# Performance work log

Measured on AMD Instinct MI355X. Metric: run time of the kernel, lower is better.

The kernel has to match this reference:

```python
import jax, jax.numpy as jnp
import numpy as np

N_NODES = 100000


def setup_inputs() -> dict:
    key = jax.random.key(0)
    k1, k2, k3 = jax.random.split(key, 3)
    x = jax.random.normal(k1, (N_NODES, 128), dtype=jnp.float32)
    edge_index = jax.random.randint(k2, (2, 1600000), 0, N_NODES, dtype=jnp.int64)
    # PyG GCNConv internal Linear (glorot init approximated by scaled normal), bias zeros
    W = jax.random.normal(k3, (128, 128), dtype=jnp.float32) * (1.0 / np.sqrt(128.0))
    b = jnp.zeros((128,), dtype=jnp.float32)
    return {"x": x, "edge_index": edge_index, "W": W, "b": b}


def gcn_conv(x, edge_index, W, b):
    N = x.shape[0]
    # add self loops
    loop = jnp.arange(N, dtype=edge_index.dtype)
    src = jnp.concatenate([edge_index[0], loop])  # message sources
    dst = jnp.concatenate([edge_index[1], loop])  # aggregation targets
    # symmetric normalization D^{-1/2} (A + I) D^{-1/2}; degree counted at dst (PyG default)
    ones = jnp.ones(src.shape[0], dtype=x.dtype)
    deg = jax.ops.segment_sum(ones, dst, num_segments=N)
    deg_inv_sqrt = jnp.where(deg > 0, jax.lax.rsqrt(jnp.maximum(deg, 1.0)), 0.0)
    norm = deg_inv_sqrt[src] * deg_inv_sqrt[dst]  # [E+N]
    h = x @ W  # [N, out]
    msgs = h[src] * norm[:, None]  # gather + scale, [E+N, out]
    agg = jax.ops.segment_sum(msgs, dst, num_segments=N)  # scatter-add
    return agg + b


def reference(x, edge_index, W, b):
    # GCNConvSC: residual + GCNConv
    return x + gcn_conv(x, edge_index, W, b)
```

## Files before the change

kernel.cpp:

```cpp
#include <hip/hip_runtime.h>


typedef __attribute__((ext_vector_type(8))) short short8;
typedef __attribute__((ext_vector_type(4))) float floatx4;

__device__ inline unsigned bf16rne(float f) {
    unsigned u = __builtin_bit_cast(unsigned, f);
    return (u + 0x7FFFu + ((u >> 16) & 1u)) >> 16;
}
__device__ inline unsigned pack2(float lo, float hi) {
    return bf16rne(lo) | (bf16rne(hi) << 16);
}
__device__ inline float bflo(unsigned u) { return __builtin_bit_cast(float, u << 16); }
__device__ inline float bfhi(unsigned u) { return __builtin_bit_cast(float, u & 0xFFFF0000u); }

#define NPB   128
#define MAXNB 1024
#define SRCB  17
#define SRCMASK ((1u << SRCB) - 1u)

__global__ void k_cvt(const float* __restrict__ x, const float* __restrict__ dis,
                      char* __restrict__ outc, int N) {
    int t = blockIdx.x * blockDim.x + threadIdx.x;
    if (t >= N * 16) return;
    int r = t >> 4, g = t & 15;
    float d = dis[r];
    const float* p = x + (size_t)r * 128 + g * 8;
    float4 a = *(const float4*)p;
    float4 c = *(const float4*)(p + 4);
    uint4 v;
    v.x = pack2(d * a.x, d * a.y); v.y = pack2(d * a.z, d * a.w);
    v.z = pack2(d * c.x, d * c.y); v.w = pack2(d * c.z, d * c.w);
    *(uint4*)(outc + (size_t)r * 512 + 256 + g * 16) = v;
}

__global__ __launch_bounds__(256) void k_hist(const int* __restrict__ dst,
                                              int* __restrict__ hist,
                                              int E, int NB, int NBLK, int chunk) {
    __shared__ int h[MAXNB];
    int tid = threadIdx.x, b = blockIdx.x;
    for (int i = tid; i < NB; i += 256) h[i] = 0;
    __syncthreads();
    int e0 = b * chunk, e1 = min(e0 + chunk, E);
    for (int e = e0 + tid; e < e1; e += 256) atomicAdd(&h[dst[e] >> 7], 1);
    __syncthreads();
    for (int k = tid; k < NB; k += 256) hist[(size_t)k * NBLK + b] = h[k];
}

__global__ __launch_bounds__(256) void k_part(const int* __restrict__ a,
                                              int* __restrict__ part, int M) {
    __shared__ int sums[256];
    int tid = threadIdx.x;
    int base = blockIdx.x * 1024 + tid * 4;
    int s = 0;
#pragma unroll
    for (int k = 0; k < 4; ++k) { int i = base + k; if (i < M) s += a[i]; }
    sums[tid] = s;
    __syncthreads();
    for (int off = 128; off > 0; off >>= 1) {
        if (tid < off) sums[tid] += sums[tid + off];
        __syncthreads();
    }
    if (tid == 0) part[blockIdx.x] = sums[0];
}

__global__ __launch_bounds__(256) void k_mid(int* __restrict__ part,
                                             int* __restrict__ ptrN,
                                             int nblk, int E) {
    __shared__ int s[256];
    int tid = threadIdx.x;
    s[tid] = (tid < nblk) ? part[tid] : 0;
    __syncthreads();
    for (int off = 1; off < 256; off <<= 1) {
        int v = (tid >= off) ? s[tid - off] : 0;
        __syncthreads();
        s[tid] += v;
        __syncthreads();
    }
    if (tid < nblk) part[tid] = tid ? s[tid - 1] : 0;
    if (tid == 0) ptrN[0] = E;
}

__global__ __launch_bounds__(256) void k_applyg(const int* __restrict__ a,
                                                const int* __restrict__ part,
                                                int* __restrict__ out, int M) {
    __shared__ int sums[256];
    int tid = threadIdx.x;
    int base = blockIdx.x * 1024 + tid * 4;
    int c[4];
    int s = 0;
#pragma unroll
    for (int k = 0; k < 4; ++k) {
        int i = base + k;
        c[k] = (i < M) ? a[i] : 0;
        s += c[k];
    }
    sums[tid] = s;
    __syncthreads();
    for (int off = 1; off < 256; off <<= 1) {
        int v = (tid >= off) ? sums[tid - off] : 0;
        __syncthreads();
        sums[tid] += v;
        __syncthreads();
    }
    int run = part[blockIdx.x] + (tid ? sums[tid - 1] : 0);
#pragma unroll
    for (int k = 0; k < 4; ++k) {
        int i = base + k;
        if (i < M) { out[i] = run; run += c[k]; }
    }
}

__global__ __launch_bounds__(256) void k_scat(const int* __restrict__ ei,
                                              const int* __restrict__ base,
                                              unsigned* __restrict__ packed,
                                              int E, int NB, int NBLK, int chunk) {
    __shared__ int fill[MAXNB];
    int tid = threadIdx.x, b = blockIdx.x;
    for (int k = tid; k < NB; k += 256) fill[k] = base[(size_t)k * NBLK + b];
    __syncthreads();
    int e0 = b * chunk, e1 = min(e0 + chunk, E);
    for (int e = e0 + tid; e < e1; e += 256) {
        int s = ei[e];
        int d = ei[E + e];
        int pos = atomicAdd(&fill[d >> 7], 1);
        packed[pos] = (unsigned)s | ((unsigned)(d & (NPB - 1)) << SRCB);
    }
}

__global__ __launch_bounds__(256) void k_sort(const unsigned* __restrict__ packed,
                                              const int* __restrict__ base,
                                              int* __restrict__ csr_src,
                                              int* __restrict__ ptr,
                                              float* __restrict__ dis,
                                              int E, int NB, int NBLK, int N) {
    __shared__ int cnt[NPB], scn[NPB], fill[NPB];
    int tid = threadIdx.x, k = blockIdx.x;
    int s0 = base[(size_t)k * NBLK];
    int s1 = (k + 1 < NB) ? base[(size_t)(k + 1) * NBLK] : E;
    if (tid < NPB) cnt[tid] = 0;
    __syncthreads();
    for (int j = s0 + tid; j < s1; j += 256) atomicAdd(&cnt[packed[j] >> SRCB], 1);
    __syncthreads();
    if (tid < NPB) scn[tid] = cnt[tid];
    __syncthreads();
    for (int off = 1; off < NPB; off <<= 1) {
        int v = (tid < NPB && tid >= off) ? scn[tid - off] : 0;
        __syncthreads();
        if (tid < NPB) scn[tid] += v;
        __syncthreads();
    }
    if (tid < NPB) {
        int excl = scn[tid] - cnt[tid];
        fill[tid] = excl;
        int gn = k * NPB + tid;
        if (gn < N) {
            ptr[gn] = s0 + excl;
            dis[gn] = rsqrtf((float)(cnt[tid] + 1));
        }
    }
    __syncthreads();
    for (int j = s0 + tid; j < s1; j += 256) {
        unsigned p = packed[j];
        int loc = atomicAdd(&fill[p >> SRCB], 1);
        csr_src[s0 + loc] = (int)(p & SRCMASK);
    }
}

#define ACC8(v)                         \
    do {                                \
        acc[0] += bflo((v).x);          \
        acc[1] += bfhi((v).x);          \
        acc[2] += bflo((v).y);          \
        acc[3] += bfhi((v).y);          \
        acc[4] += bflo((v).z);          \
        acc[5] += bfhi((v).z);          \
        acc[6] += bflo((v).w);          \
        acc[7] += bfhi((v).w);          \
    } while (0)

__global__ __launch_bounds__(256) void k_gather(char* __restrict__ outc,
                                                const int* __restrict__ csr_src,
                                                const int* __restrict__ ptr,
                                                const float* __restrict__ dis,
                                                int N) {
    int lane = threadIdx.x & 63;
    int q = lane >> 4, sub = lane & 15;
    int node = (blockIdx.x * blockDim.x + threadIdx.x) >> 6;
    if (node >= N) return;
    int lo = ptr[node], hi = ptr[node + 1];
    float dd = dis[node];
    const char* xb = outc + 256 + (size_t)sub * 16;

    float acc[8] = {0.f, 0.f, 0.f, 0.f, 0.f, 0.f, 0.f, 0.f};

    if (q == 0) {
        uint4 v = *(const uint4*)(xb + (size_t)node * 512);
        ACC8(v);
    }
    int j = lo + q;
    for (; j + 12 < hi; j += 16) {
        int s0 = csr_src[j];
        int s1 = csr_src[j + 4];
        int s2 = csr_src[j + 8];
        int s3 = csr_src[j + 12];
        uint4 v0 = *(const uint4*)(xb + (size_t)s0 * 512);
        uint4 v1 = *(const uint4*)(xb + (size_t)s1 * 512);
        uint4 v2 = *(const uint4*)(xb + (size_t)s2 * 512);
        uint4 v3 = *(const uint4*)(xb + (size_t)s3 * 512);
        ACC8(v0);
        ACC8(v1);
        ACC8(v2);
        ACC8(v3);
    }
    for (; j + 4 < hi; j += 8) {
        int s0 = csr_src[j];
        int s1 = csr_src[j + 4];
        uint4 v0 = *(const uint4*)(xb + (size_t)s0 * 512);
        uint4 v1 = *(const uint4*)(xb + (size_t)s1 * 512);
        ACC8(v0);
        ACC8(v1);
    }
    if (j < hi) {
        int s = csr_src[j];
        uint4 v = *(const uint4*)(xb + (size_t)s * 512);
        ACC8(v);
    }
#pragma unroll
    for (int i = 0; i < 8; ++i) {
        acc[i] += __shfl_xor(acc[i], 16);
        acc[i] += __shfl_xor(acc[i], 32);
    }
    if (q == 0) {
        uint4 o;
        o.x = pack2(dd * acc[0], dd * acc[1]);
        o.y = pack2(dd * acc[2], dd * acc[3]);
        o.z = pack2(dd * acc[4], dd * acc[5]);
        o.w = pack2(dd * acc[6], dd * acc[7]);
        *(uint4*)(outc + (size_t)node * 512 + sub * 16) = o;
    }
}

__global__ __launch_bounds__(256) void k_gemm(const float* __restrict__ x,
                                              const float* __restrict__ W,
                                              const float* __restrict__ bias,
                                              float* __restrict__ out, int N) {
    __shared__ short Wt[128 * 136];
    int tid = threadIdx.x;
    for (int i = tid; i < 8192; i += 256) {
        int n = i & 127, k2 = i >> 7;
        float w0 = W[(size_t)(2 * k2) * 128 + n];
        float w1 = W[(size_t)(2 * k2 + 1) * 128 + n];
        *(unsigned*)(Wt + (size_t)n * 136 + 2 * k2) = pack2(w0, w1);
    }
    __syncthreads();

    int lane = tid & 63, wv = tid >> 6;
    int quad = lane >> 4, l16 = lane & 15;
    size_t rowb = (size_t)blockIdx.x * 128 + wv * 32;
    const char* aggc = (const char*)out;

    floatx4 acc[2][8];
#pragma unroll
    for (int rt = 0; rt < 2; ++rt)
#pragma unroll
        for (int c = 0; c < 8; ++c) acc[rt][c] = (floatx4)0.0f;

    size_t r0 = rowb + l16;      if (r0 >= (size_t)N) r0 = N - 1;
    size_t r1 = rowb + 16 + l16; if (r1 >= (size_t)N) r1 = N - 1;

    for (int ks = 0; ks < 4; ++ks) {
        int koff = (quad * 8 + ks * 32) * 2;
        short8 a0 = *(const short8*)(aggc + r0 * 512 + koff);
        short8 a1 = *(const short8*)(aggc + r1 * 512 + koff);
#pragma unroll
        for (int c = 0; c < 8; ++c) {
            short8 bf = *(const short8*)(Wt + (size_t)(c * 16 + l16) * 136 + quad * 8 + ks * 32);
            acc[0][c] = __builtin_amdgcn_mfma_f32_16x16x32_bf16(a0, bf, acc[0][c], 0, 0, 0);
            acc[1][c] = __builtin_amdgcn_mfma_f32_16x16x32_bf16(a1, bf, acc[1][c], 0, 0, 0);
        }
    }

#pragma unroll
    for (int rt = 0; rt < 2; ++rt) {
#pragma unroll
        for (int c = 0; c < 8; ++c) {
            float bb = bias[c * 16 + l16];
#pragma unroll
            for (int r = 0; r < 4; ++r) {
                size_t row = rowb + rt * 16 + quad * 4 + r;
                if (row < (size_t)N) {
                    size_t idx = row * 128 + c * 16 + l16;
                    out[idx] = x[idx] + acc[rt][c][r] + bb;
                }
            }
        }
    }
}

extern "C" void kernel_launch(void* const* d_in, const int* in_sizes, int n_in,
                              void* d_out, int out_size, void* d_ws, size_t ws_size,
                              hipStream_t stream) {
    const float* x  = (const float*)d_in[0];
    const int*   ei = (const int*)d_in[1];
    const float* W  = (const float*)d_in[2];
    const float* b  = (const float*)d_in[3];
    float* out = (float*)d_out;

    int N = in_sizes[0] / 128;
    int E = in_sizes[1] / 2;
    int NB = (N + NPB - 1) / NPB;

    int chunk = 6144;
    int NBLK, M, nscan;
    size_t need;
    for (;;) {
        NBLK = (E + chunk - 1) / chunk;
        M    = NB * NBLK;
        nscan = (M + 1023) / 1024;
        need = (size_t)4 * ((size_t)2 * E + N + (N + 1) + (size_t)2 * M + 256);
        if (need <= ws_size || chunk >= 16384) break;
        chunk = 16384;
    }

    char* w = (char*)d_ws;
    unsigned* packed = (unsigned*)w; w += (size_t)E * 4;
    int*   csr_src = (int*)w;   w += (size_t)E * 4;
    float* dis     = (float*)w; w += (size_t)N * 4;
    int*   ptr     = (int*)w;   w += (size_t)(N + 1) * 4;
    int*   hist    = (int*)w;   w += (size_t)M * 4;
    int*   base    = (int*)w;   w += (size_t)M * 4;
    int*   part    = (int*)w;

    k_hist<<<NBLK, 256, 0, stream>>>(ei + E, hist, E, NB, NBLK, chunk);
    k_part<<<nscan, 256, 0, stream>>>(hist, part, M);
    k_mid<<<1, 256, 0, stream>>>(part, ptr + N, nscan, E);
    k_applyg<<<nscan, 256, 0, stream>>>(hist, part, base, M);
    k_scat<<<NBLK, 256, 0, stream>>>(ei, base, packed, E, NB, NBLK, chunk);
    k_sort<<<NB, 256, 0, stream>>>(packed, base, csr_src, ptr, dis, E, NB, NBLK, N);
    k_cvt<<<(N * 16 + 255) / 256, 256, 0, stream>>>(x, dis, (char*)out, N);
    k_gather<<<((size_t)N * 64 + 255) / 256, 256, 0, stream>>>((char*)out, csr_src, ptr, dis, N);
    k_gemm<<<(N + 127) / 128, 256, 0, stream>>>(x, W, b, out, N);
}
```

Measured before the change: 245.9 us.

## Replace per-block histogram scan with global bucket totals and atomic fill reservation

Instead of writing a per-block histogram matrix (NB x NBLK) and scanning it with three kernels, each histogram block atomically accumulates into a global per-bucket total, one single-block kernel scans the buckets, and the scatter kernel recomputes its local histogram and reserves ranges with global atomics. This removes the large histogram matrix traffic and two kernel launches. In exchange the scatter kernel reads dst twice, and the order of edges within a bucket becomes nondeterministic, though the later per-node sort still groups them by destination.

```diff
diff --git a/kernel.cpp b/kernel.cpp
--- a/kernel.cpp
+++ b/kernel.cpp
@@ -14,6 +14,8 @@
 __device__ inline float bflo(unsigned u) { return __builtin_bit_cast(float, u << 16); }
 __device__ inline float bfhi(unsigned u) { return __builtin_bit_cast(float, u & 0xFFFF0000u); }
 
+#define HCHUNK 6144
+#define SCHUNK 12288
 #define NPB   128
 #define MAXNB 1024
 #define SRCB  17
@@ -34,65 +36,35 @@
     *(uint4*)(outc + (size_t)r * 512 + 256 + g * 16) = v;
 }
 
-__global__ __launch_bounds__(256) void k_hist(const int* __restrict__ dst,
-                                              int* __restrict__ hist,
-                                              int E, int NB, int NBLK, int chunk) {
+__global__ __launch_bounds__(256) void k_hist2(const int* __restrict__ dst,
+                                               int* __restrict__ tot,
+                                               int E, int NB) {
     __shared__ int h[MAXNB];
     int tid = threadIdx.x, b = blockIdx.x;
     for (int i = tid; i < NB; i += 256) h[i] = 0;
     __syncthreads();
-    int e0 = b * chunk, e1 = min(e0 + chunk, E);
+    int e0 = b * HCHUNK, e1 = min(e0 + HCHUNK, E);
     for (int e = e0 + tid; e < e1; e += 256) atomicAdd(&h[dst[e] >> 7], 1);
     __syncthreads();
-    for (int k = tid; k < NB; k += 256) hist[(size_t)k * NBLK + b] = h[k];
-}
-
-__global__ __launch_bounds__(256) void k_part(const int* __restrict__ a,
-                                              int* __restrict__ part, int M) {
+    for (int k = tid; k < NB; k += 256) {
+        int v = h[k];
+        if (v) atomicAdd(&tot[k], v);
+    }
+}
+
+__global__ __launch_bounds__(256) void k_scan(const int* __restrict__ tot,
+                                              int* __restrict__ gstart,
+                                              int* __restrict__ gfill,
+                                              int* __restrict__ ptrN,
+                                              int NB, int E) {
     __shared__ int sums[256];
     int tid = threadIdx.x;
-    int base = blockIdx.x * 1024 + tid * 4;
-    int s = 0;
-#pragma unroll
-    for (int k = 0; k < 4; ++k) { int i = base + k; if (i < M) s += a[i]; }
-    sums[tid] = s;
-    __syncthreads();
-    for (int off = 128; off > 0; off >>= 1) {
-        if (tid < off) sums[tid] += sums[tid + off];
-        __syncthreads();
-    }
-    if (tid == 0) part[blockIdx.x] = sums[0];
-}
-
-__global__ __launch_bounds__(256) void k_mid(int* __restrict__ part,
-                                             int* __restrict__ ptrN,
-                                             int nblk, int E) {
-    __shared__ int s[256];
-    int tid = threadIdx.x;
-    s[tid] = (tid < nblk) ? part[tid] : 0;
-    __syncthreads();
-    for (int off = 1; off < 256; off <<= 1) {
-        int v = (tid >= off) ? s[tid - off] : 0;
-        __syncthreads();
-        s[tid] += v;
-        __syncthreads();
-    }
-    if (tid < nblk) part[tid] = tid ? s[tid - 1] : 0;
-    if (tid == 0) ptrN[0] = E;
-}
-
-__global__ __launch_bounds__(256) void k_applyg(const int* __restrict__ a,
-                                                const int* __restrict__ part,
-                                                int* __restrict__ out, int M) {
-    __shared__ int sums[256];
-    int tid = threadIdx.x;
-    int base = blockIdx.x * 1024 + tid * 4;
     int c[4];
     int s = 0;
 #pragma unroll
     for (int k = 0; k < 4; ++k) {
-        int i = base + k;
-        c[k] = (i < M) ? a[i] : 0;
+        int i = tid * 4 + k;
+        c[k] = (i < NB) ? tot[i] : 0;
         s += c[k];
     }
     sums[tid] = s;
@@ -103,41 +75,51 @@
         sums[tid] += v;
         __syncthreads();
     }
-    int run = part[blockIdx.x] + (tid ? sums[tid - 1] : 0);
+    int run = tid ? sums[tid - 1] : 0;
 #pragma unroll
     for (int k = 0; k < 4; ++k) {
-        int i = base + k;
-        if (i < M) { out[i] = run; run += c[k]; }
-    }
+        int i = tid * 4 + k;
+        if (i < NB) { gstart[i] = run; gfill[i] = run; run += c[k]; }
+    }
+    if (tid == 0) { gstart[NB] = E; ptrN[0] = E; }
 }
 
 __global__ __launch_bounds__(256) void k_scat(const int* __restrict__ ei,
-                                              const int* __restrict__ base,
+                                              int* __restrict__ gfill,
                                               unsigned* __restrict__ packed,
-                                              int E, int NB, int NBLK, int chunk) {
+                                              int E, int NB) {
+    __shared__ int h[MAXNB];
     __shared__ int fill[MAXNB];
     int tid = threadIdx.x, b = blockIdx.x;
-    for (int k = tid; k < NB; k += 256) fill[k] = base[(size_t)k * NBLK + b];
-    __syncthreads();
-    int e0 = b * chunk, e1 = min(e0 + chunk, E);
+    const int* dst = ei + E;
+    for (int i = tid; i < NB; i += 256) h[i] = 0;
+    __syncthreads();
+    int e0 = b * SCHUNK, e1 = min(e0 + SCHUNK, E);
+    for (int e = e0 + tid; e < e1; e += 256) atomicAdd(&h[dst[e] >> 7], 1);
+    __syncthreads();
+    for (int k = tid; k < NB; k += 256) {
+        int v = h[k];
+        fill[k] = v ? atomicAdd(&gfill[k], v) : 0;
+    }
+    __syncthreads();
     for (int e = e0 + tid; e < e1; e += 256) {
         int s = ei[e];
-        int d = ei[E + e];
+        int d = dst[e];
         int pos = atomicAdd(&fill[d >> 7], 1);
         packed[pos] = (unsigned)s | ((unsigned)(d & (NPB - 1)) << SRCB);
     }
 }
 
 __global__ __launch_bounds__(256) void k_sort(const unsigned* __restrict__ packed,
-                                              const int* __restrict__ base,
+                                              const int* __restrict__ gstart,
                                               int* __restrict__ csr_src,
                                               int* __restrict__ ptr,
                                               float* __restrict__ dis,
-                                              int E, int NB, int NBLK, int N) {
+                                              int NB, int N) {
     __shared__ int cnt[NPB], scn[NPB], fill[NPB];
     int tid = threadIdx.x, k = blockIdx.x;
-    int s0 = base[(size_t)k * NBLK];
-    int s1 = (k + 1 < NB) ? base[(size_t)(k + 1) * NBLK] : E;
+    int s0 = gstart[k];
+    int s1 = gstart[k + 1];
     if (tid < NPB) cnt[tid] = 0;
     __syncthreads();
     for (int j = s0 + tid; j < s1; j += 256) atomicAdd(&cnt[packed[j] >> SRCB], 1);
@@ -310,34 +292,23 @@
     int N = in_sizes[0] / 128;
     int E = in_sizes[1] / 2;
     int NB = (N + NPB - 1) / NPB;
-
-    int chunk = 6144;
-    int NBLK, M, nscan;
-    size_t need;
-    for (;;) {
-        NBLK = (E + chunk - 1) / chunk;
-        M    = NB * NBLK;
-        nscan = (M + 1023) / 1024;
-        need = (size_t)4 * ((size_t)2 * E + N + (N + 1) + (size_t)2 * M + 256);
-        if (need <= ws_size || chunk >= 16384) break;
-        chunk = 16384;
-    }
+    int NBH = (E + HCHUNK - 1) / HCHUNK;
+    int NBS = (E + SCHUNK - 1) / SCHUNK;
 
     char* w = (char*)d_ws;
     unsigned* packed = (unsigned*)w; w += (size_t)E * 4;
     int*   csr_src = (int*)w;   w += (size_t)E * 4;
     float* dis     = (float*)w; w += (size_t)N * 4;
     int*   ptr     = (int*)w;   w += (size_t)(N + 1) * 4;
-    int*   hist    = (int*)w;   w += (size_t)M * 4;
-    int*   base    = (int*)w;   w += (size_t)M * 4;
-    int*   part    = (int*)w;
-
-    k_hist<<<NBLK, 256, 0, stream>>>(ei + E, hist, E, NB, NBLK, chunk);
-    k_part<<<nscan, 256, 0, stream>>>(hist, part, M);
-    k_mid<<<1, 256, 0, stream>>>(part, ptr + N, nscan, E);
-    k_applyg<<<nscan, 256, 0, stream>>>(hist, part, base, M);
-    k_scat<<<NBLK, 256, 0, stream>>>(ei, base, packed, E, NB, NBLK, chunk);
-    k_sort<<<NB, 256, 0, stream>>>(packed, base, csr_src, ptr, dis, E, NB, NBLK, N);
+    int*   tot     = (int*)w;   w += (size_t)NB * 4;
+    int*   gstart  = (int*)w;   w += (size_t)(NB + 1) * 4;
+    int*   gfill   = (int*)w;
+
+    hipMemsetAsync(tot, 0, (size_t)NB * 4, stream);
+    k_hist2<<<NBH, 256, 0, stream>>>(ei + E, tot, E, NB);
+    k_scan<<<1, 256, 0, stream>>>(tot, gstart, gfill, ptr + N, NB, E);
+    k_scat<<<NBS, 256, 0, stream>>>(ei, gfill, packed, E, NB);
+    k_sort<<<NB, 256, 0, stream>>>(packed, gstart, csr_src, ptr, dis, NB, N);
     k_cvt<<<(N * 16 + 255) / 256, 256, 0, stream>>>(x, dis, (char*)out, N);
     k_gather<<<((size_t)N * 64 + 255) / 256, 256, 0, stream>>>((char*)out, csr_src, ptr, dis, N);
     k_gemm<<<(N + 127) / 128, 256, 0, stream>>>(x, W, b, out, N);
```

Result: slower. 265.8 us (+8.1%).
